# Performance work log

Hardware: AMD Instinct MI355X
Metric: run time of the kernel (lower is better)

The kernel has to match this reference:

```python
import jax, jax.numpy as jnp
import numpy as np

N = 8192          # n_nodes
E = 262144        # n_edges (avg degree 32)
F_IN, H1, H2, H3, OUT6 = 512, 256, 128, 64, 6


def setup_inputs() -> dict:
    key = jax.random.key(0)
    ks = jax.random.split(key, 12)
    x = jax.random.normal(ks[0], (N, F_IN), dtype=jnp.float32)
    adj_rows = jax.random.randint(ks[1], (E,), 0, N, dtype=jnp.int32)
    adj_cols = jax.random.randint(ks[2], (E,), 0, N, dtype=jnp.int32)
    adj_vals = jax.random.uniform(ks[3], (E,), dtype=jnp.float32)
    s = 0.05  # small init scale
    W1 = jax.random.normal(ks[4], (F_IN, H1), dtype=jnp.float32) * s
    W2 = jax.random.normal(ks[5], (H1, H2), dtype=jnp.float32) * s
    W3 = jax.random.normal(ks[6], (H1, H2), dtype=jnp.float32) * s
    dense_W = jax.random.normal(ks[7], (H2, H3), dtype=jnp.float32) * s
    dense_b = jax.random.normal(ks[8], (H3,), dtype=jnp.float32) * s
    dense1_W = jax.random.normal(ks[9], (H3, OUT6), dtype=jnp.float32) * s
    dense1_b = jax.random.normal(ks[10], (OUT6,), dtype=jnp.float32) * s
    return {"x": x, "adj_rows": adj_rows, "adj_cols": adj_cols, "adj_vals": adj_vals,
            "W1": W1, "W2": W2, "W3": W3,
            "dense_W": dense_W, "dense_b": dense_b,
            "dense1_W": dense1_W, "dense1_b": dense1_b}


def reference(x, adj_rows, adj_cols, adj_vals, W1, W2, W3,
              dense_W, dense_b, dense1_W, dense1_b):
    n = x.shape[0]

    def spmm(support):  # sparse [N,N] @ dense [N,D] via COO gather/segment-sum
        gathered = adj_vals[:, None] * support[adj_cols]  # [E, D]
        return jax.ops.segment_sum(gathered, adj_rows, num_segments=n)

    # eval mode: dropout = identity
    hidden1 = jax.nn.relu(spmm(x @ W1))          # gc1, act=relu
    mu0 = spmm(hidden1 @ W2)                     # gc2, act=identity
    logvar0 = spmm(hidden1 @ W3)                 # gc3, act=identity
    # LinearNet.forward never applies its activation -> plain affine
    mu = mu0 @ dense_W + dense_b                 # [N, H3]
    logvar = logvar0 @ dense_W + dense_b         # [N, H3]
    z = mu                                       # reparameterize in eval mode
    adj_rec = z @ z.T                            # InnerProductDecoder, act=identity
    out6 = z @ dense1_W + dense1_b               # dense1, [N, 6]
    return (adj_rec, out6, mu, logvar)
```

## Files before the change

kernel.cpp:

```cpp
#include <hip/hip_runtime.h>
#include <hip/hip_bf16.h>

#define N_NODES 8192
#define N_EDGES 262144

typedef __attribute__((ext_vector_type(8))) short short8;
typedef __attribute__((ext_vector_type(4))) float f32x4;

__device__ __forceinline__ unsigned short f2bf(float f) {
    unsigned int u = __float_as_uint(f);
    u = (u + 0x7fffu + ((u >> 16) & 1u)) >> 16;
    return (unsigned short)u;
}
__device__ __forceinline__ float bf2f(unsigned short h) {
    return __uint_as_float((unsigned int)h << 16);
}

__global__ void k_scan(const int* __restrict__ counts, int* __restrict__ offs) {
    __shared__ int part[1024];
    int t = threadIdx.x;
    int base = t * 8;
    int loc[8];
    int s = 0;
#pragma unroll
    for (int i = 0; i < 8; i++) { loc[i] = s; s += counts[base + i]; }
    part[t] = s;
    __syncthreads();
    for (int off = 1; off < 1024; off <<= 1) {
        int v = (t >= off) ? part[t - off] : 0;
        __syncthreads();
        part[t] += v;
        __syncthreads();
    }
    int prev = (t == 0) ? 0 : part[t - 1];
#pragma unroll
    for (int i = 0; i < 8; i++) offs[base + i] = prev + loc[i];
    if (t == 1023) offs[N_NODES] = part[1023];
}

__global__ void k_scatter(const int* __restrict__ rows, const int* __restrict__ colsIn,
                          const float* __restrict__ valsIn, const int* __restrict__ offs,
                          int* __restrict__ cursor, int* __restrict__ colsOut,
                          float* __restrict__ valsOut) {
    int e = blockIdx.x * 256 + threadIdx.x;
    if (e >= N_EDGES) return;
    int r = rows[e];
    int p = atomicAdd(&cursor[r], 1);
    int idx = offs[r] + p;
    colsOut[idx] = colsIn[e];
    valsOut[idx] = valsIn[e];
}

__global__ void k_prep(const int* __restrict__ rows, int* __restrict__ counts,
                       const float* __restrict__ x, ushort* __restrict__ xh,
                       const float* __restrict__ W1, ushort* __restrict__ W1t,
                       const float* __restrict__ W2, const float* __restrict__ W3,
                       ushort* __restrict__ W23t,
                       const float* __restrict__ dW, ushort* __restrict__ Wdt) {
    int b = blockIdx.x, t = threadIdx.x;
    if (b < 1024) {
        atomicAdd(&counts[rows[b * 256 + t]], 1);
    } else if (b < 5120) {
        int i = (b - 1024) * 256 + t;
        float4 v = ((const float4*)x)[i];
        ((ushort4*)xh)[i] = make_ushort4(f2bf(v.x), f2bf(v.y), f2bf(v.z), f2bf(v.w));
    } else if (b < 5632) {
        int i = (b - 5120) * 256 + t;
        int k = i >> 8, n = i & 255;
        W1t[n * 512 + k] = f2bf(W1[i]);
    } else if (b < 5888) {
        int i = (b - 5632) * 256 + t;
        int n = i >> 8, k = i & 255;
        float v = (n < 128) ? W2[k * 128 + n] : W3[k * 128 + (n - 128)];
        W23t[i] = f2bf(v);
    } else {
        int i = (b - 5888) * 256 + t;
        int j = i >> 7, k = i & 127;
        Wdt[i] = f2bf(dW[k * 64 + j]);
    }
}

__global__ __launch_bounds__(128) void k_gemm_mfma(const ushort* __restrict__ A,
                                                   const ushort* __restrict__ Bt,
                                                   ushort* __restrict__ C,
                                                   int K, int ldc) {
    int t = threadIdx.x;
    int lane = t & 63;
    int w = t >> 6;
    int I = blockIdx.y * 128 + w * 64;
    int J = blockIdx.x * 64;
    int r = lane & 15;
    int koff = (lane >> 4) * 8;
    const ushort* Ab = A + (size_t)(I + r) * K + koff;
    const ushort* Bb = Bt + (size_t)(J + r) * K + koff;
    size_t rs = (size_t)16 * K;

    short8 a0[4], b0[4], a1[4], b1[4];
#pragma unroll
    for (int m = 0; m < 4; m++) {
        a0[m] = *(const short8*)(Ab + m * rs);
        b0[m] = *(const short8*)(Bb + m * rs);
    }
    f32x4 acc[4][4];
#pragma unroll
    for (int m = 0; m < 4; m++)
#pragma unroll
        for (int n = 0; n < 4; n++) acc[m][n] = (f32x4){0.f, 0.f, 0.f, 0.f};

    int nk = K >> 5;
    for (int kt = 0; kt < nk; kt += 2) {
        int o1 = (kt + 1) << 5;
#pragma unroll
        for (int m = 0; m < 4; m++) {
            a1[m] = *(const short8*)(Ab + m * rs + o1);
            b1[m] = *(const short8*)(Bb + m * rs + o1);
        }
#pragma unroll
        for (int m = 0; m < 4; m++)
#pragma unroll
            for (int n = 0; n < 4; n++)
                acc[m][n] = __builtin_amdgcn_mfma_f32_16x16x32_bf16(a0[m], b0[n], acc[m][n], 0, 0, 0);
        if (kt + 2 < nk) {
            int o2 = (kt + 2) << 5;
#pragma unroll
            for (int m = 0; m < 4; m++) {
                a0[m] = *(const short8*)(Ab + m * rs + o2);
                b0[m] = *(const short8*)(Bb + m * rs + o2);
            }
        }
#pragma unroll
        for (int m = 0; m < 4; m++)
#pragma unroll
            for (int n = 0; n < 4; n++)
                acc[m][n] = __builtin_amdgcn_mfma_f32_16x16x32_bf16(a1[m], b1[n], acc[m][n], 0, 0, 0);
    }

    int crow = (lane >> 4) * 4;
    int ccol = lane & 15;
#pragma unroll
    for (int m = 0; m < 4; m++)
#pragma unroll
        for (int rg = 0; rg < 4; rg++) {
            size_t row = (size_t)(I + m * 16 + crow + rg);
#pragma unroll
            for (int n = 0; n < 4; n++)
                C[row * ldc + J + n * 16 + ccol] = f2bf(acc[m][n][rg]);
        }
}

__global__ __launch_bounds__(256) void k_spmm_v2(const int* __restrict__ offs,
                                                 const int* __restrict__ cols,
                                                 const float* __restrict__ vals,
                                                 const ushort* __restrict__ in,
                                                 ushort* __restrict__ out, int relu) {
    int w = threadIdx.x >> 6;
    int lane = threadIdx.x & 63;
    int row = blockIdx.x * 4 + w;
    int colo = lane * 4;
    int i = offs[row], e = offs[row + 1];
    float4 acc = make_float4(0.f, 0.f, 0.f, 0.f);
    int c = 0;
    float v = 0.f;
    if (i < e) { c = cols[i]; v = vals[i]; }
    while (i < e) {
        int cn = 0;
        float vn = 0.f;
        if (i + 1 < e) { cn = cols[i + 1]; vn = vals[i + 1]; }
        ushort4 u = *(const ushort4*)&in[(size_t)c * 256 + colo];
        acc.x += v * bf2f(u.x);
        acc.y += v * bf2f(u.y);
        acc.z += v * bf2f(u.z);
        acc.w += v * bf2f(u.w);
        c = cn; v = vn; ++i;
    }
    if (relu) {
        acc.x = fmaxf(acc.x, 0.f); acc.y = fmaxf(acc.y, 0.f);
        acc.z = fmaxf(acc.z, 0.f); acc.w = fmaxf(acc.w, 0.f);
    }
    *(ushort4*)&out[(size_t)row * 256 + colo] =
        make_ushort4(f2bf(acc.x), f2bf(acc.y), f2bf(acc.z), f2bf(acc.w));
}

__global__ __launch_bounds__(256) void k_dense_mfma(const ushort* __restrict__ A,
                                                    const ushort* __restrict__ Wdt,
                                                    const float* __restrict__ bias,
                                                    float* __restrict__ mu,
                                                    float* __restrict__ logvar,
                                                    ushort* __restrict__ Zh) {
    int t = threadIdx.x;
    int lane = t & 63;
    int w = t >> 6;
    int I = blockIdx.x * 256 + w * 64;
    int r = lane & 15;
    int koff = (lane >> 4) * 8;

    f32x4 acc[4][4];
#pragma unroll
    for (int m = 0; m < 4; m++)
#pragma unroll
        for (int n = 0; n < 4; n++) acc[m][n] = (f32x4){0.f, 0.f, 0.f, 0.f};

#pragma unroll
    for (int kk = 0; kk < 4; kk++) {
        short8 a[4], b[4];
#pragma unroll
        for (int m = 0; m < 4; m++)
            a[m] = *(const short8*)(A + (size_t)(I + m * 16 + r) * 128 + kk * 32 + koff);
#pragma unroll
        for (int n = 0; n < 4; n++)
            b[n] = *(const short8*)(Wdt + (size_t)(n * 16 + r) * 128 + kk * 32 + koff);
#pragma unroll
        for (int m = 0; m < 4; m++)
#pragma unroll
            for (int n = 0; n < 4; n++)
                acc[m][n] = __builtin_amdgcn_mfma_f32_16x16x32_bf16(a[m], b[n], acc[m][n], 0, 0, 0);
    }

    int crow = (lane >> 4) * 4;
    int ccol = lane & 15;
#pragma unroll
    for (int m = 0; m < 4; m++)
#pragma unroll
        for (int rg = 0; rg < 4; rg++) {
            int vrow = I + m * 16 + crow + rg;
            int nr = vrow >> 1;
#pragma unroll
            for (int n = 0; n < 4; n++) {
                int col = n * 16 + ccol;
                float val = acc[m][n][rg] + bias[col];
                if (vrow & 1) {
                    logvar[(size_t)nr * 64 + col] = val;
                } else {
                    mu[(size_t)nr * 64 + col] = val;
                    Zh[(size_t)nr * 64 + col] = f2bf(val);
                }
            }
        }
}

__global__ __launch_bounds__(256) void k_out6(const float* __restrict__ Z,
                                              const float* __restrict__ W,
                                              const float* __restrict__ b,
                                              float* __restrict__ out) {
    __shared__ float sW[384];
    int t = threadIdx.x;
    for (int i = t; i < 384; i += 256) sW[i] = W[i];
    __syncthreads();
    int row = blockIdx.x * 256 + t;
    float acc[6];
#pragma unroll
    for (int j = 0; j < 6; j++) acc[j] = b[j];
    for (int k = 0; k < 64; k++) {
        float zv = Z[(size_t)row * 64 + k];
#pragma unroll
        for (int j = 0; j < 6; j++) acc[j] += zv * sW[k * 6 + j];
    }
#pragma unroll
    for (int j = 0; j < 6; j++) out[(size_t)row * 6 + j] = acc[j];
}

__global__ __launch_bounds__(256) void k_zzt_mfma(const ushort* __restrict__ Zh,
                                                  float* __restrict__ C) {
    int t = threadIdx.x;
    int lane = t & 63;
    int w = t >> 6;
    int I = blockIdx.y * 128 + (w >> 1) * 64;
    int J = blockIdx.x * 128 + (w & 1) * 64;
    int r = lane & 15;
    int koff = (lane >> 4) * 8;

    short8 a[4][2], b[4][2];
#pragma unroll
    for (int m = 0; m < 4; m++) {
#pragma unroll
        for (int kk = 0; kk < 2; kk++) {
            a[m][kk] = *(const short8*)(Zh + (size_t)(I + m * 16 + r) * 64 + kk * 32 + koff);
            b[m][kk] = *(const short8*)(Zh + (size_t)(J + m * 16 + r) * 64 + kk * 32 + koff);
        }
    }
    f32x4 acc[4][4];
#pragma unroll
    for (int m = 0; m < 4; m++)
#pragma unroll
        for (int n = 0; n < 4; n++) acc[m][n] = (f32x4){0.f, 0.f, 0.f, 0.f};

#pragma unroll
    for (int kk = 0; kk < 2; kk++)
#pragma unroll
        for (int m = 0; m < 4; m++)
#pragma unroll
            for (int n = 0; n < 4; n++)
                acc[m][n] = __builtin_amdgcn_mfma_f32_16x16x32_bf16(a[m][kk], b[n][kk],
                                                                    acc[m][n], 0, 0, 0);

    int crow = (lane >> 4) * 4;
    int ccol = lane & 15;
#pragma unroll
    for (int m = 0; m < 4; m++)
#pragma unroll
        for (int rg = 0; rg < 4; rg++) {
            size_t row = (size_t)(I + m * 16 + crow + rg);
#pragma unroll
            for (int n = 0; n < 4; n++)
                C[row * 8192 + J + n * 16 + ccol] = acc[m][n][rg];
        }
}

extern "C" void kernel_launch(void* const* d_in, const int* in_sizes, int n_in,
                              void* d_out, int out_size, void* d_ws, size_t ws_size,
                              hipStream_t stream) {
    const float* x        = (const float*)d_in[0];
    const int*   adj_rows = (const int*)d_in[1];
    const int*   adj_cols = (const int*)d_in[2];
    const float* adj_vals = (const float*)d_in[3];
    const float* W1       = (const float*)d_in[4];
    const float* W2       = (const float*)d_in[5];
    const float* W3       = (const float*)d_in[6];
    const float* dense_W  = (const float*)d_in[7];
    const float* dense_b  = (const float*)d_in[8];
    const float* dense1_W = (const float*)d_in[9];
    const float* dense1_b = (const float*)d_in[10];

    char* p = (char*)d_ws;
    int* counts  = (int*)p;    p += 8192 * 4;
    int* cursor  = (int*)p;    p += 8192 * 4;
    int* offs    = (int*)p;    p += 8224 * 4;
    int* scol    = (int*)p;    p += (size_t)N_EDGES * 4;
    float* sval  = (float*)p;  p += (size_t)N_EDGES * 4;
    ushort* xh   = (ushort*)p; p += (size_t)8192 * 512 * 2;
    ushort* W1t  = (ushort*)p; p += (size_t)256 * 512 * 2;
    ushort* W23t = (ushort*)p; p += (size_t)256 * 256 * 2;
    ushort* Wdt  = (ushort*)p; p += (size_t)64 * 128 * 2;
    ushort* XW1h = (ushort*)p; p += (size_t)8192 * 256 * 2;
    ushort* Hidh = (ushort*)p; p += (size_t)8192 * 256 * 2;
    ushort* Tbh  = (ushort*)p; p += (size_t)8192 * 256 * 2;
    ushort* Mbh  = (ushort*)p; p += (size_t)8192 * 256 * 2;
    ushort* Zh   = (ushort*)p; p += (size_t)8192 * 64 * 2;

    float* out     = (float*)d_out;
    float* adj_rec = out;
    float* out6    = out + (size_t)8192 * 8192;
    float* mu      = out6 + (size_t)8192 * 6;
    float* logvar  = mu + (size_t)8192 * 64;

    hipMemsetAsync(counts, 0, 2 * 8192 * 4, stream);
    k_prep<<<5920, 256, 0, stream>>>(adj_rows, counts, x, xh, W1, W1t, W2, W3, W23t,
                                     dense_W, Wdt);
    k_scan<<<1, 1024, 0, stream>>>(counts, offs);
    k_scatter<<<N_EDGES / 256, 256, 0, stream>>>(adj_rows, adj_cols, adj_vals, offs, cursor,
                                                 scol, sval);

    k_gemm_mfma<<<dim3(4, 64), 128, 0, stream>>>(xh, W1t, XW1h, 512, 256);
    k_spmm_v2<<<2048, 256, 0, stream>>>(offs, scol, sval, XW1h, Hidh, 1);
    k_gemm_mfma<<<dim3(4, 64), 128, 0, stream>>>(Hidh, W23t, Tbh, 256, 256);
    k_spmm_v2<<<2048, 256, 0, stream>>>(offs, scol, sval, Tbh, Mbh, 0);
    k_dense_mfma<<<64, 256, 0, stream>>>(Mbh, Wdt, dense_b, mu, logvar, Zh);
    k_out6<<<32, 256, 0, stream>>>(mu, dense1_W, dense1_b, out6);
    k_zzt_mfma<<<dim3(64, 64), 256, 0, stream>>>(Zh, adj_rec);
}
```

Before: 418.8 us.

## Fold dense layer into GCN weights and fuse second SpMM with outputs

Precomputes W2·dense_W and W3·dense_W in the prep kernel, so the second GEMM produces 128 columns instead of 256 and the second SpMM gathers half the data. The final SpMM then adds the bias and writes mu, logvar, Zh and the 6-wide output in one pass, removing the separate dense and out6 kernels. The ZZ^T store is changed to vector writes of the transposed tile, relying on the output being symmetric. The weight folding adds a serial 128-term dot product per prep thread and rounds the combined weights to bf16, which slightly changes numerics.

Measured after the change: 447.6 us. 1.07x slower.

```diff
diff --git a/kernel.cpp b/kernel.cpp
--- a/kernel.cpp
+++ b/kernel.cpp
@@ -55,8 +55,7 @@
                        const float* __restrict__ x, ushort* __restrict__ xh,
                        const float* __restrict__ W1, ushort* __restrict__ W1t,
                        const float* __restrict__ W2, const float* __restrict__ W3,
-                       ushort* __restrict__ W23t,
-                       const float* __restrict__ dW, ushort* __restrict__ Wdt) {
+                       const float* __restrict__ dW, ushort* __restrict__ W23dt) {
     int b = blockIdx.x, t = threadIdx.x;
     if (b < 1024) {
         atomicAdd(&counts[rows[b * 256 + t]], 1);
@@ -68,15 +67,15 @@
         int i = (b - 5120) * 256 + t;
         int k = i >> 8, n = i & 255;
         W1t[n * 512 + k] = f2bf(W1[i]);
-    } else if (b < 5888) {
+    } else {
         int i = (b - 5632) * 256 + t;
         int n = i >> 8, k = i & 255;
-        float v = (n < 128) ? W2[k * 128 + n] : W3[k * 128 + (n - 128)];
-        W23t[i] = f2bf(v);
-    } else {
-        int i = (b - 5888) * 256 + t;
-        int j = i >> 7, k = i & 127;
-        Wdt[i] = f2bf(dW[k * 64 + j]);
+        const float* src = (n < 64) ? W2 : W3;
+        int nn = n & 63;
+        float acc = 0.f;
+        for (int j = 0; j < 128; j++)
+            acc += src[k * 128 + j] * dW[j * 64 + nn];
+        W23dt[i] = f2bf(acc);
     }
 }
 
@@ -152,7 +151,7 @@
                                                  const int* __restrict__ cols,
                                                  const float* __restrict__ vals,
                                                  const ushort* __restrict__ in,
-                                                 ushort* __restrict__ out, int relu) {
+                                                 ushort* __restrict__ out) {
     int w = threadIdx.x >> 6;
     int lane = threadIdx.x & 63;
     int row = blockIdx.x * 4 + w;
@@ -173,90 +172,64 @@
         acc.w += v * bf2f(u.w);
         c = cn; v = vn; ++i;
     }
-    if (relu) {
-        acc.x = fmaxf(acc.x, 0.f); acc.y = fmaxf(acc.y, 0.f);
-        acc.z = fmaxf(acc.z, 0.f); acc.w = fmaxf(acc.w, 0.f);
-    }
+    acc.x = fmaxf(acc.x, 0.f); acc.y = fmaxf(acc.y, 0.f);
+    acc.z = fmaxf(acc.z, 0.f); acc.w = fmaxf(acc.w, 0.f);
     *(ushort4*)&out[(size_t)row * 256 + colo] =
         make_ushort4(f2bf(acc.x), f2bf(acc.y), f2bf(acc.z), f2bf(acc.w));
 }
 
-__global__ __launch_bounds__(256) void k_dense_mfma(const ushort* __restrict__ A,
-                                                    const ushort* __restrict__ Wdt,
-                                                    const float* __restrict__ bias,
-                                                    float* __restrict__ mu,
-                                                    float* __restrict__ logvar,
-                                                    ushort* __restrict__ Zh) {
+__global__ __launch_bounds__(256) void k_spmm_fin(const int* __restrict__ offs,
+                                                  const int* __restrict__ cols,
+                                                  const float* __restrict__ vals,
+                                                  const ushort* __restrict__ U,
+                                                  const float* __restrict__ bias,
+                                                  const float* __restrict__ W6,
+                                                  const float* __restrict__ b6,
+                                                  float* __restrict__ mu,
+                                                  float* __restrict__ logvar,
+                                                  ushort* __restrict__ Zh,
+                                                  float* __restrict__ out6) {
+    __shared__ float smu[4][64];
+    __shared__ float sW6[384];
     int t = threadIdx.x;
-    int lane = t & 63;
-    int w = t >> 6;
-    int I = blockIdx.x * 256 + w * 64;
-    int r = lane & 15;
-    int koff = (lane >> 4) * 8;
-
-    f32x4 acc[4][4];
-#pragma unroll
-    for (int m = 0; m < 4; m++)
-#pragma unroll
-        for (int n = 0; n < 4; n++) acc[m][n] = (f32x4){0.f, 0.f, 0.f, 0.f};
-
-#pragma unroll
-    for (int kk = 0; kk < 4; kk++) {
-        short8 a[4], b[4];
-#pragma unroll
-        for (int m = 0; m < 4; m++)
-            a[m] = *(const short8*)(A + (size_t)(I + m * 16 + r) * 128 + kk * 32 + koff);
-#pragma unroll
-        for (int n = 0; n < 4; n++)
-            b[n] = *(const short8*)(Wdt + (size_t)(n * 16 + r) * 128 + kk * 32 + koff);
-#pragma unroll
-        for (int m = 0; m < 4; m++)
-#pragma unroll
-            for (int n = 0; n < 4; n++)
-                acc[m][n] = __builtin_amdgcn_mfma_f32_16x16x32_bf16(a[m], b[n], acc[m][n], 0, 0, 0);
-    }
-
-    int crow = (lane >> 4) * 4;
-    int ccol = lane & 15;
-#pragma unroll
-    for (int m = 0; m < 4; m++)
-#pragma unroll
-        for (int rg = 0; rg < 4; rg++) {
-            int vrow = I + m * 16 + crow + rg;
-            int nr = vrow >> 1;
-#pragma unroll
-            for (int n = 0; n < 4; n++) {
-                int col = n * 16 + ccol;
-                float val = acc[m][n][rg] + bias[col];
-                if (vrow & 1) {
-                    logvar[(size_t)nr * 64 + col] = val;
-                } else {
-                    mu[(size_t)nr * 64 + col] = val;
-                    Zh[(size_t)nr * 64 + col] = f2bf(val);
-                }
-            }
-        }
-}
-
-__global__ __launch_bounds__(256) void k_out6(const float* __restrict__ Z,
-                                              const float* __restrict__ W,
-                                              const float* __restrict__ b,
-                                              float* __restrict__ out) {
-    __shared__ float sW[384];
-    int t = threadIdx.x;
-    for (int i = t; i < 384; i += 256) sW[i] = W[i];
+    for (int i = t; i < 384; i += 256) sW6[i] = W6[i];
+    int w = t >> 6, lane = t & 63;
+    int row = blockIdx.x * 4 + w;
+    int colo = lane * 2;
+    int i = offs[row], e = offs[row + 1];
+    float2 acc = make_float2(0.f, 0.f);
+    int c = 0;
+    float v = 0.f;
+    if (i < e) { c = cols[i]; v = vals[i]; }
+    while (i < e) {
+        int cn = 0;
+        float vn = 0.f;
+        if (i + 1 < e) { cn = cols[i + 1]; vn = vals[i + 1]; }
+        ushort2 u = *(const ushort2*)&U[(size_t)c * 128 + colo];
+        acc.x += v * bf2f(u.x);
+        acc.y += v * bf2f(u.y);
+        c = cn; v = vn; ++i;
+    }
+    int bc = colo & 63;
+    acc.x += bias[bc];
+    acc.y += bias[bc + 1];
+    if (lane < 32) {
+        *(float2*)&mu[(size_t)row * 64 + colo] = acc;
+        ushort2 h;
+        h.x = f2bf(acc.x);
+        h.y = f2bf(acc.y);
+        *(ushort2*)&Zh[(size_t)row * 64 + colo] = h;
+        smu[w][colo] = acc.x;
+        smu[w][colo + 1] = acc.y;
+    } else {
+        *(float2*)&logvar[(size_t)row * 64 + (colo - 64)] = acc;
+    }
     __syncthreads();
-    int row = blockIdx.x * 256 + t;
-    float acc[6];
-#pragma unroll
-    for (int j = 0; j < 6; j++) acc[j] = b[j];
-    for (int k = 0; k < 64; k++) {
-        float zv = Z[(size_t)row * 64 + k];
-#pragma unroll
-        for (int j = 0; j < 6; j++) acc[j] += zv * sW[k * 6 + j];
-    }
-#pragma unroll
-    for (int j = 0; j < 6; j++) out[(size_t)row * 6 + j] = acc[j];
+    if (lane < 6) {
+        float a6 = b6[lane];
+        for (int k = 0; k < 64; k++) a6 += smu[w][k] * sW6[k * 6 + lane];
+        out6[(size_t)row * 6 + lane] = a6;
+    }
 }
 
 __global__ __launch_bounds__(256) void k_zzt_mfma(const ushort* __restrict__ Zh,
@@ -298,11 +271,9 @@
 #pragma unroll
     for (int m = 0; m < 4; m++)
 #pragma unroll
-        for (int rg = 0; rg < 4; rg++) {
-            size_t row = (size_t)(I + m * 16 + crow + rg);
-#pragma unroll
-            for (int n = 0; n < 4; n++)
-                C[row * 8192 + J + n * 16 + ccol] = acc[m][n][rg];
+        for (int n = 0; n < 4; n++) {
+            size_t orow = (size_t)(J + n * 16 + ccol);
+            *(f32x4*)&C[orow * 8192 + I + m * 16 + crow] = acc[m][n];
         }
 }
 
@@ -322,20 +293,18 @@
     const float* dense1_b = (const float*)d_in[10];
 
     char* p = (char*)d_ws;
-    int* counts  = (int*)p;    p += 8192 * 4;
-    int* cursor  = (int*)p;    p += 8192 * 4;
-    int* offs    = (int*)p;    p += 8224 * 4;
-    int* scol    = (int*)p;    p += (size_t)N_EDGES * 4;
-    float* sval  = (float*)p;  p += (size_t)N_EDGES * 4;
-    ushort* xh   = (ushort*)p; p += (size_t)8192 * 512 * 2;
-    ushort* W1t  = (ushort*)p; p += (size_t)256 * 512 * 2;
-    ushort* W23t = (ushort*)p; p += (size_t)256 * 256 * 2;
-    ushort* Wdt  = (ushort*)p; p += (size_t)64 * 128 * 2;
-    ushort* XW1h = (ushort*)p; p += (size_t)8192 * 256 * 2;
-    ushort* Hidh = (ushort*)p; p += (size_t)8192 * 256 * 2;
-    ushort* Tbh  = (ushort*)p; p += (size_t)8192 * 256 * 2;
-    ushort* Mbh  = (ushort*)p; p += (size_t)8192 * 256 * 2;
-    ushort* Zh   = (ushort*)p; p += (size_t)8192 * 64 * 2;
+    int* counts   = (int*)p;    p += 8192 * 4;
+    int* cursor   = (int*)p;    p += 8192 * 4;
+    int* offs     = (int*)p;    p += 8224 * 4;
+    int* scol     = (int*)p;    p += (size_t)N_EDGES * 4;
+    float* sval   = (float*)p;  p += (size_t)N_EDGES * 4;
+    ushort* xh    = (ushort*)p; p += (size_t)8192 * 512 * 2;
+    ushort* W1t   = (ushort*)p; p += (size_t)256 * 512 * 2;
+    ushort* W23dt = (ushort*)p; p += (size_t)128 * 256 * 2;
+    ushort* XW1h  = (ushort*)p; p += (size_t)8192 * 256 * 2;
+    ushort* Hidh  = (ushort*)p; p += (size_t)8192 * 256 * 2;
+    ushort* Uh    = (ushort*)p; p += (size_t)8192 * 128 * 2;
+    ushort* Zh    = (ushort*)p; p += (size_t)8192 * 64 * 2;
 
     float* out     = (float*)d_out;
     float* adj_rec = out;
@@ -344,17 +313,16 @@
     float* logvar  = mu + (size_t)8192 * 64;
 
     hipMemsetAsync(counts, 0, 2 * 8192 * 4, stream);
-    k_prep<<<5920, 256, 0, stream>>>(adj_rows, counts, x, xh, W1, W1t, W2, W3, W23t,
-                                     dense_W, Wdt);
+    k_prep<<<5760, 256, 0, stream>>>(adj_rows, counts, x, xh, W1, W1t, W2, W3,
+                                     dense_W, W23dt);
     k_scan<<<1, 1024, 0, stream>>>(counts, offs);
     k_scatter<<<N_EDGES / 256, 256, 0, stream>>>(adj_rows, adj_cols, adj_vals, offs, cursor,
                                                  scol, sval);
 
     k_gemm_mfma<<<dim3(4, 64), 128, 0, stream>>>(xh, W1t, XW1h, 512, 256);
-    k_spmm_v2<<<2048, 256, 0, stream>>>(offs, scol, sval, XW1h, Hidh, 1);
-    k_gemm_mfma<<<dim3(4, 64), 128, 0, stream>>>(Hidh, W23t, Tbh, 256, 256);
-    k_spmm_v2<<<2048, 256, 0, stream>>>(offs, scol, sval, Tbh, Mbh, 0);
-    k_dense_mfma<<<64, 256, 0, stream>>>(Mbh, Wdt, dense_b, mu, logvar, Zh);
-    k_out6<<<32, 256, 0, stream>>>(mu, dense1_W, dense1_b, out6);
+    k_spmm_v2<<<2048, 256, 0, stream>>>(offs, scol, sval, XW1h, Hidh);
+    k_gemm_mfma<<<dim3(2, 64), 128, 0, stream>>>(Hidh, W23dt, Uh, 256, 128);
+    k_spmm_fin<<<2048, 256, 0, stream>>>(offs, scol, sval, Uh, dense_b, dense1_W, dense1_b,
+                                         mu, logvar, Zh, out6);
     k_zzt_mfma<<<dim3(64, 64), 256, 0, stream>>>(Zh, adj_rec);
 }
```
